# Kernel optimization log

Hardware: AMD Instinct MI355X
Metric: run time of the kernel (lower is better)

Reference implementation:

```python
import jax, jax.numpy as jnp
import numpy as np

DILATION = 6
KS = 3
N = KS * KS  # 9 kernel sample points
PAD = 1      # zero padding inside DeformConv2d
EPS = 1e-5


def conv2d(x, w, b=None, padding=0):
    out = jax.lax.conv_general_dilated(
        x, w, window_strides=(1, 1),
        padding=[(padding, padding), (padding, padding)],
        dimension_numbers=('NCHW', 'OIHW', 'NCHW'))
    if b is not None:
        out = out + b[None, :, None, None]
    return out


def batchnorm_train(x, gamma, beta):
    # training-mode BN (module default): batch statistics over (N,H,W)
    mean = x.mean(axis=(0, 2, 3), keepdims=True)
    var = x.var(axis=(0, 2, 3), keepdims=True)
    return gamma[None, :, None, None] * (x - mean) * jax.lax.rsqrt(var + EPS) + beta[None, :, None, None]


def deform_conv(x, p_w, p_b, m_w, m_b, d_w, d_b, w):
    b, c, h, wd = x.shape
    offset = conv2d(x, p_w, p_b, padding=1)                 # (b, 2N, h, w)
    m = jax.nn.sigmoid(conv2d(x, m_w, m_b, padding=1))      # (b, N, h, w) modulation
    s = 2.0 * jax.nn.sigmoid(conv2d(x, d_w, d_b, padding=1))  # (b,1,h,w) adaptive dilation scale (=1 at logit 0)
    xp = jnp.pad(x, ((0, 0), (0, 0), (PAD, PAD), (PAD, PAD)))
    Hp, Wp = h + 2 * PAD, wd + 2 * PAD
    # kernel grid p_n, row-major (kh, kw) to match conv weight layout
    rng = jnp.arange(-(KS - 1) // 2, (KS - 1) // 2 + 1, dtype=x.dtype)
    pn_x, pn_y = jnp.meshgrid(rng, rng, indexing='ij')
    pn_x, pn_y = pn_x.reshape(-1), pn_y.reshape(-1)          # (N,)
    # base sampling positions (offset by PAD into padded map)
    p0_x = jnp.arange(1, h + 1, dtype=x.dtype)[:, None, None]    # (h,1,1)
    p0_y = jnp.arange(1, wd + 1, dtype=x.dtype)[None, :, None]   # (1,w,1)
    off = offset.transpose(0, 2, 3, 1)   # (b,h,w,2N)
    s_ = s.transpose(0, 2, 3, 1)         # (b,h,w,1)
    px = p0_x + DILATION * s_ * pn_x + off[..., :N]   # (b,h,w,N)
    py = p0_y + DILATION * s_ * pn_y + off[..., N:]
    fx, fy = jnp.floor(px), jnp.floor(py)
    qx_lt = jnp.clip(fx, 0, Hp - 1).astype(jnp.int32)
    qy_lt = jnp.clip(fy, 0, Wp - 1).astype(jnp.int32)
    qx_rb = jnp.clip(fx + 1, 0, Hp - 1).astype(jnp.int32)
    qy_rb = jnp.clip(fy + 1, 0, Wp - 1).astype(jnp.int32)
    pxc = jnp.clip(px, 0, Hp - 1)
    pyc = jnp.clip(py, 0, Wp - 1)
    g_lt = (1 + (qx_lt - pxc)) * (1 + (qy_lt - pyc))
    g_rb = (1 - (qx_rb - pxc)) * (1 - (qy_rb - pyc))
    g_lb = (1 + (qx_lt - pxc)) * (1 - (qy_rb - pyc))
    g_rt = (1 - (qx_rb - pxc)) * (1 + (qy_lt - pyc))

    def gather(qx, qy):
        idx = (qx * Wp + qy).reshape(b, 1, -1)                    # (b,1,h*w*N)
        xf = xp.reshape(b, c, Hp * Wp)
        out = jnp.take_along_axis(xf, jnp.broadcast_to(idx, (b, c, idx.shape[-1])), axis=2)
        return out.reshape(b, c, h, wd, N)

    x_off = (g_lt[:, None] * gather(qx_lt, qy_lt)
             + g_rb[:, None] * gather(qx_rb, qy_rb)
             + g_lb[:, None] * gather(qx_lt, qy_rb)
             + g_rt[:, None] * gather(qx_rb, qy_lt))
    x_off = x_off * m.transpose(0, 2, 3, 1)[:, None]              # modulation
    # final 3x3 conv over gathered samples == contraction over (c, N)
    return jnp.einsum('bchwn,ocn->bohw', x_off, w.reshape(w.shape[0], c, N))


def setup_inputs() -> dict:
    key = jax.random.key(0)
    ks = jax.random.split(key, 12)
    cin, c1, c2 = 512, 256, 64
    b, h, w = 2, 96, 96
    def rn(k, shape, scale):
        return jax.random.normal(k, shape, dtype=jnp.float32) * scale
    return {
        'x': rn(ks[0], (b, cin, h, w), 1.0),
        'bn1_g': jnp.ones((cin,), jnp.float32),
        'bn1_b': jnp.zeros((cin,), jnp.float32),
        'conv1_w': rn(ks[1], (c1, cin, 1, 1), (1.0 / cin) ** 0.5),
        'conv1_b': jnp.zeros((c1,), jnp.float32),
        'bn2_g': jnp.ones((c1,), jnp.float32),
        'bn2_b': jnp.zeros((c1,), jnp.float32),
        'p_w': rn(ks[2], (2 * N, c1, 3, 3), 0.01),
        'p_b': jnp.zeros((2 * N,), jnp.float32),
        'm_w': rn(ks[3], (N, c1, 3, 3), 0.01),
        'm_b': jnp.zeros((N,), jnp.float32),
        'd_w': rn(ks[4], (1, c1, 3, 3), 0.01),
        'd_b': jnp.zeros((1,), jnp.float32),
        'dconv_w': rn(ks[5], (c2, c1, 3, 3), (1.0 / (c1 * 9)) ** 0.5),
    }


def reference(x, bn1_g, bn1_b, conv1_w, conv1_b, bn2_g, bn2_b,
              p_w, p_b, m_w, m_b, d_w, d_b, dconv_w):
    f = jax.nn.relu(batchnorm_train(x, bn1_g, bn1_b))
    f = conv2d(f, conv1_w, conv1_b)
    f = batchnorm_train(f, bn2_g, bn2_b)
    return deform_conv(f, p_w, p_b, m_w, m_b, d_w, d_b, dconv_w)
```

## Files before the change

kernel.cpp:

```cpp
#include <hip/hip_runtime.h>
#include <hip/hip_bf16.h>
#include <math.h>

#define BATCH 2
#define CIN 512
#define C1 256
#define C2 64
#define HH 96
#define WW 96
#define HWSZ 9216
#define NPIX 18432
#define HP 98
#define WP 98

typedef __attribute__((ext_vector_type(8))) short bf16x8;
typedef __attribute__((ext_vector_type(4))) short bf16x4;
typedef __attribute__((ext_vector_type(4))) float f32x4;
typedef __attribute__((ext_vector_type(4))) unsigned int u32x4;
typedef __attribute__((ext_vector_type(2))) unsigned int u32x2;
typedef unsigned short u16;
typedef unsigned int u32;

__device__ __forceinline__ float bfu2f(u16 u) {
  u32 v = ((u32)u) << 16; return __builtin_bit_cast(float, v);
}
__device__ __forceinline__ u16 f2bfu(float f) {
  return __builtin_bit_cast(u16, __float2bfloat16(f));
}
__device__ __forceinline__ float rd_any(const void* p, size_t i, int fl) {
  return fl ? bfu2f(((const u16*)p)[i]) : ((const float*)p)[i];
}
__device__ __forceinline__ int get_fl(const u32* g1raw) {
  return g1raw[0] != 0x3F800000u;
}
__device__ __forceinline__ bf16x8 lds_frag(const u16* p) {
  bf16x4 lo = *(const bf16x4*)p;
  bf16x4 hi = *(const bf16x4*)(p + 4);
  bf16x8 r;
  r[0] = lo[0]; r[1] = lo[1]; r[2] = lo[2]; r[3] = lo[3];
  r[4] = hi[0]; r[5] = hi[1]; r[6] = hi[2]; r[7] = hi[3];
  return r;
}
__device__ __forceinline__ void split4(const f32x4& v, u32x2& ph, u32x2& pl) {
  u16 h0 = f2bfu(v[0]), h1 = f2bfu(v[1]), h2 = f2bfu(v[2]), h3 = f2bfu(v[3]);
  u16 l0 = f2bfu(v[0] - bfu2f(h0)), l1 = f2bfu(v[1] - bfu2f(h1));
  u16 l2 = f2bfu(v[2] - bfu2f(h2)), l3 = f2bfu(v[3] - bfu2f(h3));
  ph = (u32x2){(u32)h0 | ((u32)h1 << 16), (u32)h2 | ((u32)h3 << 16)};
  pl = (u32x2){(u32)l0 | ((u32)l1 << 16), (u32)l2 | ((u32)l3 << 16)};
}

__global__ __launch_bounds__(256) void prep_kernel(
    const void* cw, const void* pw, const void* mw, const void* dw, const void* dcw,
    const void* cb, const void* g1, const void* b1, const void* g2, const void* b2,
    const void* pb, const void* mb, const void* db,
    u16* __restrict__ W1b, u16* __restrict__ W1l,
    u16* __restrict__ Wofa, u16* __restrict__ Wofal,
    u16* __restrict__ Wab, u16* __restrict__ Wabl,
    float* __restrict__ canon, float* __restrict__ statz) {
  int e = blockIdx.x * 256 + threadIdx.x;
  if (e >= 356380) return;
  int fl = get_fl((const u32*)g1);
  if (e < 131072) {
    float v = rd_any(cw, e, fl);
    u16 h = f2bfu(v);
    W1b[e] = h; W1l[e] = f2bfu(v - bfu2f(h));
  } else if (e < 204800) {
    int i = e - 131072;
    int tap = i >> 13; int r = i & 8191; int m = r >> 8; int c = r & 255;
    float v = 0.f;
    if (m < 18)       v = rd_any(pw, (size_t)(m * 256 + c) * 9 + tap, fl);
    else if (m < 27)  v = rd_any(mw, (size_t)((m - 18) * 256 + c) * 9 + tap, fl);
    else if (m == 27) v = rd_any(dw, (size_t)c * 9 + tap, fl);
    u16 h = f2bfu(v);
    Wofa[i] = h; Wofal[i] = f2bfu(v - bfu2f(h));
  } else if (e < 352256) {
    int i = e - 204800;
    int n = i >> 14; int r = i & 16383; int o = r >> 8; int c = r & 255;
    float v = rd_any(dcw, (size_t)(o * 256 + c) * 9 + n, fl);
    u16 h = f2bfu(v);
    Wab[i] = h; Wabl[i] = f2bfu(v - bfu2f(h));
  } else if (e < 354076) {
    int i = e - 352256;
    const void* src; int off;
    if      (i < 256)  { src = cb; off = i; }
    else if (i < 768)  { src = g1; off = i - 256; }
    else if (i < 1280) { src = b1; off = i - 768; }
    else if (i < 1536) { src = g2; off = i - 1280; }
    else if (i < 1792) { src = b2; off = i - 1536; }
    else if (i < 1810) { src = pb; off = i - 1792; }
    else if (i < 1819) { src = mb; off = i - 1810; }
    else               { src = db; off = i - 1819; }
    canon[i] = rd_any(src, off, fl);
  } else {
    statz[e - 354076] = 0.f;
  }
}

__global__ __launch_bounds__(256) void bn_stats_kernel(
    const void* __restrict__ x, const float* __restrict__ gamma,
    const float* __restrict__ beta, float* __restrict__ scale,
    float* __restrict__ shift, float* __restrict__ sums, float* __restrict__ sumsq,
    int* __restrict__ cnt, const u32* __restrict__ g1raw, int force, int C) {
  int c = blockIdx.x, part = blockIdx.y, tid = threadIdx.x;
  int fl = force ? 1 : get_fl(g1raw);
  int b = part >> 1, half = part & 1;
  size_t base = ((size_t)(b * C + c)) * HWSZ + half * (HWSZ / 2);
  float s = 0.f, q = 0.f;
  if (fl) {
    const u16* p = (const u16*)x + base;
    for (int i = tid; i < 576; i += 256) {
      u32x4 U = *(const u32x4*)(p + i * 8);
      #pragma unroll
      for (int k = 0; k < 4; ++k) {
        float v0 = bfu2f((u16)(U[k] & 0xffff));
        float v1 = bfu2f((u16)(U[k] >> 16));
        s += v0 + v1; q = fmaf(v0, v0, fmaf(v1, v1, q));
      }
    }
  } else {
    const float* p = (const float*)x + base;
    for (int i = tid; i < 1152; i += 256) {
      f32x4 v = *(const f32x4*)(p + i * 4);
      #pragma unroll
      for (int k = 0; k < 4; ++k) { s += v[k]; q = fmaf(v[k], v[k], q); }
    }
  }
  __shared__ float sh[512];
  sh[tid] = s; sh[tid + 256] = q;
  __syncthreads();
  for (int off = 128; off > 0; off >>= 1) {
    if (tid < off) { sh[tid] += sh[tid + off]; sh[tid + 256] += sh[tid + 256 + off]; }
    __syncthreads();
  }
  if (tid == 0) {
    atomicAdd(&sums[c], sh[0]);
    atomicAdd(&sumsq[c], sh[256]);
    __threadfence();
    int old = atomicAdd(&cnt[c], 1);
    if (old == 3) {
      float S = atomicAdd(&sums[c], 0.f);
      float Q = atomicAdd(&sumsq[c], 0.f);
      float mean = S * (1.f / (float)NPIX);
      float var  = fmaxf(Q * (1.f / (float)NPIX) - mean * mean, 0.f);
      float sc = gamma[c] * rsqrtf(var + 1e-5f);
      scale[c] = sc;
      shift[c] = beta[c] - mean * sc;
    }
  }
}

__global__ __launch_bounds__(256) void conv1x1_kernel(
    const void* __restrict__ x, const u16* __restrict__ W1b, const u16* __restrict__ W1l,
    const float* __restrict__ cb, const float* __restrict__ scale,
    const float* __restrict__ shift, const u32* __restrict__ g1raw,
    u16* __restrict__ f1) {
  __shared__ u16 Bh[2][64][68];
  __shared__ u16 Bl[2][64][68];
  int tid = threadIdx.x;
  int fl = get_fl(g1raw);
  int bxr = blockIdx.x;
  int bx = (bxr & 7) * 36 + (bxr >> 3);
  int p0 = bx * 64;
  int co0 = blockIdx.y * 128;
  int b = p0 / HWSZ;
  int hw0 = p0 % HWSZ;
  int lane = tid & 63, wv = tid >> 6, quad = lane >> 4, mr = lane & 15;
  int m0 = co0 + wv * 32;
  f32x4 acc[2][4];
  #pragma unroll
  for (int i = 0; i < 2; ++i)
    #pragma unroll
    for (int j = 0; j < 4; ++j) acc[i][j] = (f32x4){0.f, 0.f, 0.f, 0.f};

  int spx = tid & 63, cg = tid >> 6;
  int gpx = hw0 + spx;

  float pva[8], pvb[8];
  auto ISSUE = [&](int c0) {
    #pragma unroll
    for (int j = 0; j < 8; ++j) {
      int ci = c0 + cg * 16 + j * 2;
      if (fl) {
        const u16* xb = (const u16*)x;
        pva[j] = bfu2f(xb[((size_t)(b * CIN + ci)) * HWSZ + gpx]);
        pvb[j] = bfu2f(xb[((size_t)(b * CIN + ci + 1)) * HWSZ + gpx]);
      } else {
        const float* xf = (const float*)x;
        pva[j] = xf[((size_t)(b * CIN + ci)) * HWSZ + gpx];
        pvb[j] = xf[((size_t)(b * CIN + ci + 1)) * HWSZ + gpx];
      }
    }
  };
  auto COMBINE = [&](int buf, int c0) {
    #pragma unroll
    for (int j = 0; j < 8; ++j) {
      int ci = c0 + cg * 16 + j * 2;
      float v0 = fmaxf(fmaf(pva[j], scale[ci], shift[ci]), 0.f);
      float v1 = fmaxf(fmaf(pvb[j], scale[ci + 1], shift[ci + 1]), 0.f);
      u16 h0 = f2bfu(v0), h1 = f2bfu(v1);
      u16 l0 = f2bfu(v0 - bfu2f(h0)), l1 = f2bfu(v1 - bfu2f(h1));
      *(u32*)&Bh[buf][spx][cg * 16 + j * 2] = (u32)h0 | ((u32)h1 << 16);
      *(u32*)&Bl[buf][spx][cg * 16 + j * 2] = (u32)l0 | ((u32)l1 << 16);
    }
  };

  ISSUE(0);
  COMBINE(0, 0);
  for (int c8 = 0; c8 < 8; ++c8) {
    __syncthreads();
    if (c8 < 7) ISSUE((c8 + 1) * 64);
    int bsel = c8 & 1;
    int c0 = c8 * 64;
    #pragma unroll
    for (int kk2 = 0; kk2 < 2; ++kk2) {
      int kk = kk2 * 32;
      #pragma unroll
      for (int mf = 0; mf < 2; ++mf) {
        size_t wix = (size_t)(m0 + mf * 16 + mr) * CIN + c0 + kk + quad * 8;
        bf16x8 ah = *(const bf16x8*)(W1b + wix);
        bf16x8 al = *(const bf16x8*)(W1l + wix);
        #pragma unroll
        for (int nt = 0; nt < 4; ++nt) {
          bf16x8 bl = lds_frag(&Bl[bsel][nt * 16 + mr][kk + quad * 8]);
          bf16x8 bh = lds_frag(&Bh[bsel][nt * 16 + mr][kk + quad * 8]);
          acc[mf][nt] = __builtin_amdgcn_mfma_f32_16x16x32_bf16(ah, bl, acc[mf][nt], 0, 0, 0);
          acc[mf][nt] = __builtin_amdgcn_mfma_f32_16x16x32_bf16(al, bh, acc[mf][nt], 0, 0, 0);
          acc[mf][nt] = __builtin_amdgcn_mfma_f32_16x16x32_bf16(ah, bh, acc[mf][nt], 0, 0, 0);
        }
      }
    }
    if (c8 < 7) COMBINE(bsel ^ 1, (c8 + 1) * 64);
  }
  #pragma unroll
  for (int mf = 0; mf < 2; ++mf) {
    #pragma unroll
    for (int nt = 0; nt < 4; ++nt) {
      #pragma unroll
      for (int r = 0; r < 4; ++r) {
        int co = m0 + mf * 16 + quad * 4 + r;
        f1[((size_t)(b * C1 + co)) * HWSZ + hw0 + nt * 16 + mr] = f2bfu(acc[mf][nt][r] + cb[co]);
      }
    }
  }
}

__global__ __launch_bounds__(256) void bn2pad_kernel(
    const u16* __restrict__ f1, const float* __restrict__ scale,
    const float* __restrict__ shift, float* __restrict__ xpf) {
  int bid = blockIdx.x;
  int ht = bid % 144; int ct = (bid / 144) & 3; int b = bid / 576;
  int hw0 = ht * 64, c0 = ct * 64;
  __shared__ float t[64][65];
  int tid = threadIdx.x;
  #pragma unroll
  for (int it = 0; it < 16; ++it) {
    int e = it * 256 + tid;
    int p = e & 63, ci = e >> 6;
    float v = bfu2f(f1[((size_t)(b * C1 + c0 + ci)) * HWSZ + hw0 + p]);
    t[ci][p] = fmaf(v, scale[c0 + ci], shift[c0 + ci]);
  }
  __syncthreads();
  #pragma unroll
  for (int it = 0; it < 16; ++it) {
    int e = it * 256 + tid;
    int ci = e & 63, p = e >> 6;
    int hw = hw0 + p; int h = hw / WW; int w = hw % WW;
    xpf[(((size_t)(b * HP) + h + 1) * WP + w + 1) * C1 + c0 + ci] = t[ci][p];
  }
}

__global__ __launch_bounds__(256) void init_kernel(
    const u32* __restrict__ g1raw, void* __restrict__ outv,
    float* __restrict__ oscr, float* __restrict__ opart, float* __restrict__ xpf) {
  int i = blockIdx.x * 256 + threadIdx.x;
  if (i < 1179648) {
    if (get_fl(g1raw)) { ((u16*)outv)[i] = 0; oscr[i] = 0.f; }
    else               { ((float*)outv)[i] = 0.f; }
  } else if (i < 1769472) {
    opart[i - 1179648] = 0.f;
  } else {
    int k = i - 1769472;
    int ch = k & 255; int pxi = k >> 8;
    int bb = pxi / 388; int r = pxi % 388;
    int h, w;
    if (r < 98)      { h = 0;  w = r; }
    else if (r < 196){ h = 97; w = r - 98; }
    else if (r < 292){ h = r - 196 + 1; w = 0; }
    else             { h = r - 292 + 1; w = 97; }
    xpf[(((size_t)(bb * HP) + h) * WP + w) * C1 + ch] = 0.f;
  }
}

__global__ __launch_bounds__(256) void offconv_kernel(
    const float* __restrict__ xpf, const u16* __restrict__ Wofa, const u16* __restrict__ Wofal,
    const float* __restrict__ pbc, const float* __restrict__ mbc,
    const float* __restrict__ dbc, float* __restrict__ opart) {
  __shared__ u16 Vh[2][32][68];
  __shared__ u16 Vl[2][32][68];
  int tid = threadIdx.x;
  int bxr = blockIdx.x;
  int bx = (bxr & 7) * 72 + (bxr >> 3);
  int tg = blockIdx.y;
  int p0 = bx * 32;
  int b = p0 / HWSZ;
  int hw = p0 % HWSZ; int h0 = hw / WW; int w0 = hw % WW;
  int lane = tid & 63, wv = tid >> 6, quad = lane >> 4, mr = lane & 15;
  int m0 = (wv & 1) * 16;
  int ntile = wv >> 1;
  int srow = tid >> 4;
  int scol = (tid & 15) * 4;
  f32x4 acc = (f32x4){0.f, 0.f, 0.f, 0.f};

  f32x4 pv[2];
  auto ISSUE = [&](int it) {
    int tap = tg * 3 + (it >> 2);
    int th = tap / 3, tw = tap % 3;
    int c0 = (it & 3) * 64;
    const float* base = xpf + ((size_t)(b * HP + h0 + th) * WP + (w0 + tw)) * C1;
    #pragma unroll
    for (int pass = 0; pass < 2; ++pass) {
      int px = pass * 16 + srow;
      pv[pass] = *(const f32x4*)(base + (size_t)px * C1 + c0 + scol);
    }
  };
  auto COMBINE = [&](int buf) {
    #pragma unroll
    for (int pass = 0; pass < 2; ++pass) {
      int px = pass * 16 + srow;
      u32x2 ph, pl;
      split4(pv[pass], ph, pl);
      *(u32x2*)&Vh[buf][px][scol] = ph;
      *(u32x2*)&Vl[buf][px][scol] = pl;
    }
  };

  ISSUE(0);
  COMBINE(0);
  for (int it = 0; it < 12; ++it) {
    __syncthreads();
    if (it < 11) ISSUE(it + 1);
    int bsel = it & 1;
    int tap = tg * 3 + (it >> 2);
    int c0 = (it & 3) * 64;
    #pragma unroll
    for (int kk2 = 0; kk2 < 2; ++kk2) {
      int kof = kk2 * 32 + quad * 8;
      size_t wix = (size_t)(tap * 32 + m0 + mr) * C1 + c0 + kof;
      bf16x8 ah = *(const bf16x8*)(Wofa + wix);
      bf16x8 al = *(const bf16x8*)(Wofal + wix);
      bf16x8 bl = lds_frag(&Vl[bsel][ntile * 16 + mr][kof]);
      bf16x8 bh = lds_frag(&Vh[bsel][ntile * 16 + mr][kof]);
      acc = __builtin_amdgcn_mfma_f32_16x16x32_bf16(ah, bl, acc, 0, 0, 0);
      acc = __builtin_amdgcn_mfma_f32_16x16x32_bf16(al, bh, acc, 0, 0, 0);
      acc = __builtin_amdgcn_mfma_f32_16x16x32_bf16(ah, bh, acc, 0, 0, 0);
    }
    if (it < 11) COMBINE(bsel ^ 1);
  }
  int px = ntile * 16 + mr;
  #pragma unroll
  for (int r = 0; r < 4; ++r) {
    int m = m0 + quad * 4 + r;
    if (m < 28) {
      float v = acc[r];
      if (tg == 0) v += (m < 18) ? pbc[m] : ((m < 27) ? mbc[m - 18] : dbc[0]);
      atomicAdd(&opart[(size_t)m * NPIX + p0 + px], v);
    }
  }
}

__global__ __launch_bounds__(256) void deform_kernel(
    const float* __restrict__ xpf, const u16* __restrict__ Wab, const u16* __restrict__ Wabl,
    const float* __restrict__ opart, const u32* __restrict__ g1raw,
    float* __restrict__ oscr, void* __restrict__ outv) {
  __shared__ u16   Vh[2][64][68];
  __shared__ u16   Vl[2][64][68];
  __shared__ int   smi[4][64];
  __shared__ float smw[4][64];
  int tid = threadIdx.x;
  int bxr = blockIdx.x;
  int bx = (bxr & 7) * 36 + (bxr >> 3);
  int n = blockIdx.y;
  int p0 = bx * 64;
  int b = p0 / HWSZ;
  int hw0 = p0 % HWSZ;

  if (tid < 64) {
    int p = tid;
    int bp = p0 + p;
    int hw = hw0 + p; int h = hw / WW; int w = hw % WW;
    float offx = opart[(size_t)n * NPIX + bp];
    float offy = opart[(size_t)(9 + n) * NPIX + bp];
    float mlog = opart[(size_t)(18 + n) * NPIX + bp];
    float slog = opart[(size_t)27 * NPIX + bp];
    float mm = 1.f / (1.f + expf(-mlog));
    float s  = 2.f / (1.f + expf(-slog));
    float pnx = (float)(n / 3 - 1), pny = (float)(n % 3 - 1);
    float px = (float)(h + 1) + 6.f * s * pnx + offx;
    float py = (float)(w + 1) + 6.f * s * pny + offy;
    float fx = floorf(px), fy = floorf(py);
    float qxlt = fminf(fmaxf(fx, 0.f), 97.f);
    float qylt = fminf(fmaxf(fy, 0.f), 97.f);
    float qxrb = fminf(fmaxf(fx + 1.f, 0.f), 97.f);
    float qyrb = fminf(fmaxf(fy + 1.f, 0.f), 97.f);
    float pxc = fminf(fmaxf(px, 0.f), 97.f);
    float pyc = fminf(fmaxf(py, 0.f), 97.f);
    float glt = (1.f + (qxlt - pxc)) * (1.f + (qylt - pyc));
    float grb = (1.f - (qxrb - pxc)) * (1.f - (qyrb - pyc));
    float glb = (1.f + (qxlt - pxc)) * (1.f - (qyrb - pyc));
    float grt = (1.f - (qxrb - pxc)) * (1.f + (qylt - pyc));
    int ixlt = (int)qxlt, iylt = (int)qylt, ixrb = (int)qxrb, iyrb = (int)qyrb;
    int base = b * (HP * WP);
    smi[0][p] = base + ixlt * WP + iylt;  smw[0][p] = glt * mm;
    smi[1][p] = base + ixrb * WP + iyrb;  smw[1][p] = grb * mm;
    smi[2][p] = base + ixlt * WP + iyrb;  smw[2][p] = glb * mm;
    smi[3][p] = base + ixrb * WP + iylt;  smw[3][p] = grt * mm;
  }
  __syncthreads();

  int lane = tid & 63, wv = tid >> 6, quad = lane >> 4, mr = lane & 15;
  int m0 = wv * 16;
  int srow = tid >> 4;
  int scol = (tid & 15) * 4;
  f32x4 acc[4];
  #pragma unroll
  for (int i = 0; i < 4; ++i) acc[i] = (f32x4){0.f, 0.f, 0.f, 0.f};

  f32x4 pv[4][4];
  auto ISSUE = [&](int c0) {
    #pragma unroll
    for (int pass = 0; pass < 4; ++pass) {
      int px = pass * 16 + srow;
      #pragma unroll
      for (int k = 0; k < 4; ++k)
        pv[pass][k] = *(const f32x4*)(xpf + (size_t)smi[k][px] * C1 + c0 + scol);
    }
  };
  auto COMBINE = [&](int buf) {
    #pragma unroll
    for (int pass = 0; pass < 4; ++pass) {
      int px = pass * 16 + srow;
      float w0 = smw[0][px], w1 = smw[1][px], w2 = smw[2][px], w3 = smw[3][px];
      f32x4 vc;
      #pragma unroll
      for (int j = 0; j < 4; ++j)
        vc[j] = fmaf(w0, pv[pass][0][j],
                fmaf(w1, pv[pass][1][j],
                fmaf(w2, pv[pass][2][j], w3 * pv[pass][3][j])));
      u32x2 ph, pl;
      split4(vc, ph, pl);
      *(u32x2*)&Vh[buf][px][scol] = ph;
      *(u32x2*)&Vl[buf][px][scol] = pl;
    }
  };

  ISSUE(0);
  COMBINE(0);
  for (int c0i = 0; c0i < 4; ++c0i) {
    __syncthreads();
    if (c0i < 3) ISSUE((c0i + 1) * 64);
    int bsel = c0i & 1;
    int c0 = c0i * 64;
    #pragma unroll
    for (int kk2 = 0; kk2 < 2; ++kk2) {
      int kof = kk2 * 32 + quad * 8;
      size_t wix = (size_t)(n * C2 + m0 + mr) * C1 + c0 + kof;
      bf16x8 ah = *(const bf16x8*)(Wab + wix);
      bf16x8 al = *(const bf16x8*)(Wabl + wix);
      #pragma unroll
      for (int nt = 0; nt < 4; ++nt) {
        bf16x8 bl = lds_frag(&Vl[bsel][nt * 16 + mr][kof]);
        bf16x8 bh = lds_frag(&Vh[bsel][nt * 16 + mr][kof]);
        acc[nt] = __builtin_amdgcn_mfma_f32_16x16x32_bf16(ah, bl, acc[nt], 0, 0, 0);
        acc[nt] = __builtin_amdgcn_mfma_f32_16x16x32_bf16(al, bh, acc[nt], 0, 0, 0);
        acc[nt] = __builtin_amdgcn_mfma_f32_16x16x32_bf16(ah, bh, acc[nt], 0, 0, 0);
      }
    }
    if (c0i < 3) COMBINE(bsel ^ 1);
  }
  int fl = get_fl(g1raw);
  float* tgt = fl ? oscr : (float*)outv;
  #pragma unroll
  for (int nt = 0; nt < 4; ++nt) {
    #pragma unroll
    for (int r = 0; r < 4; ++r) {
      int o = m0 + quad * 4 + r;
      int hw = hw0 + nt * 16 + mr;
      atomicAdd(&tgt[((size_t)(b * C2 + o)) * HWSZ + hw], acc[nt][r]);
    }
  }
}

__global__ void cvt_out_kernel(const u32* __restrict__ g1raw,
                               const float* __restrict__ oscr, void* __restrict__ outv) {
  if (!get_fl(g1raw)) return;
  int i = blockIdx.x * 256 + threadIdx.x;
  ((u16*)outv)[i] = f2bfu(oscr[i]);
}

extern "C" void kernel_launch(void* const* d_in, const int* in_sizes, int n_in,
                              void* d_out, int out_size, void* d_ws, size_t ws_size,
                              hipStream_t stream) {
  const void* x       = d_in[0];
  const void* bn1_g   = d_in[1];
  const void* bn1_b   = d_in[2];
  const void* conv1_w = d_in[3];
  const void* conv1_b = d_in[4];
  const void* bn2_g   = d_in[5];
  const void* bn2_b   = d_in[6];
  const void* p_w     = d_in[7];
  const void* p_b     = d_in[8];
  const void* m_w     = d_in[9];
  const void* m_b     = d_in[10];
  const void* d_w     = d_in[11];
  const void* d_b     = d_in[12];
  const void* dconv_w = d_in[13];
  const u32* g1raw = (const u32*)bn1_g;

  float* ws = (float*)d_ws;
  float* canon = ws + 16;
  float* cbc = canon + 0;
  float* g1c = canon + 256;
  float* b1c = canon + 768;
  float* g2c = canon + 1280;
  float* b2c = canon + 1536;
  float* pbc = canon + 1792;
  float* mbc = canon + 1810;
  float* dbc = canon + 1819;
  float* scale1 = ws + 1840;
  float* shift1 = ws + 2352;
  float* scale2 = ws + 2864;
  float* shift2 = ws + 3120;
  float* statz  = ws + 3376;
  float* sums1  = statz;
  float* sumsq1 = statz + 512;
  int*   cnt1   = (int*)(statz + 1024);
  float* sums2  = statz + 1536;
  float* sumsq2 = statz + 1792;
  int*   cnt2   = (int*)(statz + 2048);
  u16* W1b   = (u16*)(ws + 5680);
  u16* W1l   = (u16*)(ws + 71216);
  u16* Wofa  = (u16*)(ws + 136752);
  u16* Wofal = (u16*)(ws + 173616);
  u16* Wab   = (u16*)(ws + 210480);
  u16* Wabl  = (u16*)(ws + 284208);
  u16* f1    = (u16*)(ws + 357936);
  float* oscr  = ws + 357936;
  float* opart = ws + 1537584;
  float* xpf   = ws + 2717232;

  prep_kernel<<<1393, 256, 0, stream>>>(conv1_w, p_w, m_w, d_w, dconv_w,
                                        conv1_b, bn1_g, bn1_b, bn2_g, bn2_b,
                                        p_b, m_b, d_b,
                                        W1b, W1l, Wofa, Wofal, Wab, Wabl, canon, statz);
  bn_stats_kernel<<<dim3(CIN, 4), 256, 0, stream>>>(x, g1c, b1c, scale1, shift1,
                                                    sums1, sumsq1, cnt1, g1raw, 0, CIN);
  conv1x1_kernel<<<dim3(288, 2), 256, 0, stream>>>(x, W1b, W1l, cbc, scale1, shift1, g1raw, f1);
  bn_stats_kernel<<<dim3(C1, 4), 256, 0, stream>>>(f1, g2c, b2c, scale2, shift2,
                                                   sums2, sumsq2, cnt2, g1raw, 1, C1);
  bn2pad_kernel<<<1152, 256, 0, stream>>>(f1, scale2, shift2, xpf);
  init_kernel<<<7688, 256, 0, stream>>>(g1raw, d_out, oscr, opart, xpf);
  offconv_kernel<<<dim3(576, 3), 256, 0, stream>>>(xpf, Wofa, Wofal, pbc, mbc, dbc, opart);
  deform_kernel<<<dim3(288, 9), 256, 0, stream>>>(xpf, Wab, Wabl, opart, g1raw, oscr, d_out);
  cvt_out_kernel<<<4608, 256, 0, stream>>>(g1raw, oscr, d_out);
}
```

Measured before the change: 308.4 us.

## Replace atomic accumulation with per-tap-group planes and in-block tap reduction

The offset conv now writes each of its three tap-group partial sums to a separate plane, and the deform kernel adds them up on read, so no atomics or zero-init are needed. The deform kernel loops over all 9 kernel taps inside one block of 32 pixels, so it writes the final output directly in the output dtype. This removes the output zeroing, the atomicAdds and the bf16 conversion kernel. In exchange the deform kernel has a smaller pixel tile, a longer serial 36-step loop and fewer blocks (576), which may lower parallelism.

```diff
diff --git a/kernel.cpp b/kernel.cpp
--- a/kernel.cpp
+++ b/kernel.cpp
@@ -12,6 +12,7 @@
 #define NPIX 18432
 #define HP 98
 #define WP 98
+#define PLSTRIDE 516096
 
 typedef __attribute__((ext_vector_type(8))) short bf16x8;
 typedef __attribute__((ext_vector_type(4))) short bf16x4;
@@ -269,32 +270,22 @@
   }
 }
 
-__global__ __launch_bounds__(256) void init_kernel(
-    const u32* __restrict__ g1raw, void* __restrict__ outv,
-    float* __restrict__ oscr, float* __restrict__ opart, float* __restrict__ xpf) {
-  int i = blockIdx.x * 256 + threadIdx.x;
-  if (i < 1179648) {
-    if (get_fl(g1raw)) { ((u16*)outv)[i] = 0; oscr[i] = 0.f; }
-    else               { ((float*)outv)[i] = 0.f; }
-  } else if (i < 1769472) {
-    opart[i - 1179648] = 0.f;
-  } else {
-    int k = i - 1769472;
-    int ch = k & 255; int pxi = k >> 8;
-    int bb = pxi / 388; int r = pxi % 388;
-    int h, w;
-    if (r < 98)      { h = 0;  w = r; }
-    else if (r < 196){ h = 97; w = r - 98; }
-    else if (r < 292){ h = r - 196 + 1; w = 0; }
-    else             { h = r - 292 + 1; w = 97; }
-    xpf[(((size_t)(bb * HP) + h) * WP + w) * C1 + ch] = 0.f;
-  }
+__global__ __launch_bounds__(256) void init_kernel(float* __restrict__ xpf) {
+  int k = blockIdx.x * 256 + threadIdx.x;
+  int ch = k & 255; int pxi = k >> 8;
+  int bb = pxi / 388; int r = pxi % 388;
+  int h, w;
+  if (r < 98)      { h = 0;  w = r; }
+  else if (r < 196){ h = 97; w = r - 98; }
+  else if (r < 292){ h = r - 196 + 1; w = 0; }
+  else             { h = r - 292 + 1; w = 97; }
+  xpf[(((size_t)(bb * HP) + h) * WP + w) * C1 + ch] = 0.f;
 }
 
 __global__ __launch_bounds__(256) void offconv_kernel(
     const float* __restrict__ xpf, const u16* __restrict__ Wofa, const u16* __restrict__ Wofal,
     const float* __restrict__ pbc, const float* __restrict__ mbc,
-    const float* __restrict__ dbc, float* __restrict__ opart) {
+    const float* __restrict__ dbc, float* __restrict__ opart3) {
   __shared__ u16 Vh[2][32][68];
   __shared__ u16 Vl[2][32][68];
   int tid = threadIdx.x;
@@ -356,6 +347,7 @@
     }
     if (it < 11) COMBINE(bsel ^ 1);
   }
+  float* plane = opart3 + (size_t)tg * PLSTRIDE;
   int px = ntile * 16 + mr;
   #pragma unroll
   for (int r = 0; r < 4; ++r) {
@@ -363,35 +355,42 @@
     if (m < 28) {
       float v = acc[r];
       if (tg == 0) v += (m < 18) ? pbc[m] : ((m < 27) ? mbc[m - 18] : dbc[0]);
-      atomicAdd(&opart[(size_t)m * NPIX + p0 + px], v);
+      plane[(size_t)m * NPIX + p0 + px] = v;
     }
   }
 }
 
 __global__ __launch_bounds__(256) void deform_kernel(
     const float* __restrict__ xpf, const u16* __restrict__ Wab, const u16* __restrict__ Wabl,
-    const float* __restrict__ opart, const u32* __restrict__ g1raw,
-    float* __restrict__ oscr, void* __restrict__ outv) {
-  __shared__ u16   Vh[2][64][68];
-  __shared__ u16   Vl[2][64][68];
-  __shared__ int   smi[4][64];
-  __shared__ float smw[4][64];
+    const float* __restrict__ opart3, const u32* __restrict__ g1raw,
+    void* __restrict__ outv) {
+  __shared__ u16   Vh[2][32][68];
+  __shared__ u16   Vl[2][32][68];
+  __shared__ int   smi[9][4][32];
+  __shared__ float smw[9][4][32];
   int tid = threadIdx.x;
   int bxr = blockIdx.x;
-  int bx = (bxr & 7) * 36 + (bxr >> 3);
-  int n = blockIdx.y;
-  int p0 = bx * 64;
+  int bx = (bxr & 7) * 72 + (bxr >> 3);
+  int p0 = bx * 32;
   int b = p0 / HWSZ;
   int hw0 = p0 % HWSZ;
 
-  if (tid < 64) {
-    int p = tid;
+  for (int e = tid; e < 288; e += 256) {
+    int n = e >> 5;
+    int p = e & 31;
     int bp = p0 + p;
     int hw = hw0 + p; int h = hw / WW; int w = hw % WW;
-    float offx = opart[(size_t)n * NPIX + bp];
-    float offy = opart[(size_t)(9 + n) * NPIX + bp];
-    float mlog = opart[(size_t)(18 + n) * NPIX + bp];
-    float slog = opart[(size_t)27 * NPIX + bp];
+    const float* P0 = opart3;
+    const float* P1 = opart3 + PLSTRIDE;
+    const float* P2 = opart3 + 2 * PLSTRIDE;
+    size_t iox = (size_t)n * NPIX + bp;
+    size_t ioy = (size_t)(9 + n) * NPIX + bp;
+    size_t iml = (size_t)(18 + n) * NPIX + bp;
+    size_t isl = (size_t)27 * NPIX + bp;
+    float offx = P0[iox] + P1[iox] + P2[iox];
+    float offy = P0[ioy] + P1[ioy] + P2[ioy];
+    float mlog = P0[iml] + P1[iml] + P2[iml];
+    float slog = P0[isl] + P1[isl] + P2[isl];
     float mm = 1.f / (1.f + expf(-mlog));
     float s  = 2.f / (1.f + expf(-slog));
     float pnx = (float)(n / 3 - 1), pny = (float)(n % 3 - 1);
@@ -410,10 +409,10 @@
     float grt = (1.f - (qxrb - pxc)) * (1.f + (qylt - pyc));
     int ixlt = (int)qxlt, iylt = (int)qylt, ixrb = (int)qxrb, iyrb = (int)qyrb;
     int base = b * (HP * WP);
-    smi[0][p] = base + ixlt * WP + iylt;  smw[0][p] = glt * mm;
-    smi[1][p] = base + ixrb * WP + iyrb;  smw[1][p] = grb * mm;
-    smi[2][p] = base + ixlt * WP + iyrb;  smw[2][p] = glb * mm;
-    smi[3][p] = base + ixrb * WP + iylt;  smw[3][p] = grt * mm;
+    smi[n][0][p] = base + ixlt * WP + iylt;  smw[n][0][p] = glt * mm;
+    smi[n][1][p] = base + ixrb * WP + iyrb;  smw[n][1][p] = grb * mm;
+    smi[n][2][p] = base + ixlt * WP + iyrb;  smw[n][2][p] = glb * mm;
+    smi[n][3][p] = base + ixrb * WP + iylt;  smw[n][3][p] = grt * mm;
   }
   __syncthreads();
 
@@ -421,25 +420,27 @@
   int m0 = wv * 16;
   int srow = tid >> 4;
   int scol = (tid & 15) * 4;
-  f32x4 acc[4];
-  #pragma unroll
-  for (int i = 0; i < 4; ++i) acc[i] = (f32x4){0.f, 0.f, 0.f, 0.f};
-
-  f32x4 pv[4][4];
-  auto ISSUE = [&](int c0) {
-    #pragma unroll
-    for (int pass = 0; pass < 4; ++pass) {
+  f32x4 acc[2];
+  acc[0] = (f32x4){0.f, 0.f, 0.f, 0.f};
+  acc[1] = (f32x4){0.f, 0.f, 0.f, 0.f};
+
+  f32x4 pv[2][4];
+  auto ISSUE = [&](int it) {
+    int n = it >> 2; int c0 = (it & 3) * 64;
+    #pragma unroll
+    for (int pass = 0; pass < 2; ++pass) {
       int px = pass * 16 + srow;
       #pragma unroll
       for (int k = 0; k < 4; ++k)
-        pv[pass][k] = *(const f32x4*)(xpf + (size_t)smi[k][px] * C1 + c0 + scol);
+        pv[pass][k] = *(const f32x4*)(xpf + (size_t)smi[n][k][px] * C1 + c0 + scol);
     }
   };
-  auto COMBINE = [&](int buf) {
-    #pragma unroll
-    for (int pass = 0; pass < 4; ++pass) {
+  auto COMBINE = [&](int buf, int it) {
+    int n = it >> 2;
+    #pragma unroll
+    for (int pass = 0; pass < 2; ++pass) {
       int px = pass * 16 + srow;
-      float w0 = smw[0][px], w1 = smw[1][px], w2 = smw[2][px], w3 = smw[3][px];
+      float w0 = smw[n][0][px], w1 = smw[n][1][px], w2 = smw[n][2][px], w3 = smw[n][3][px];
       f32x4 vc;
       #pragma unroll
       for (int j = 0; j < 4; ++j)
@@ -454,12 +455,12 @@
   };
 
   ISSUE(0);
-  COMBINE(0);
-  for (int c0i = 0; c0i < 4; ++c0i) {
+  COMBINE(0, 0);
+  for (int it = 0; it < 36; ++it) {
     __syncthreads();
-    if (c0i < 3) ISSUE((c0i + 1) * 64);
-    int bsel = c0i & 1;
-    int c0 = c0i * 64;
+    if (it < 35) ISSUE(it + 1);
+    int bsel = it & 1;
+    int n = it >> 2; int c0 = (it & 3) * 64;
     #pragma unroll
     for (int kk2 = 0; kk2 < 2; ++kk2) {
       int kof = kk2 * 32 + quad * 8;
@@ -467,7 +468,7 @@
       bf16x8 ah = *(const bf16x8*)(Wab + wix);
       bf16x8 al = *(const bf16x8*)(Wabl + wix);
       #pragma unroll
-      for (int nt = 0; nt < 4; ++nt) {
+      for (int nt = 0; nt < 2; ++nt) {
         bf16x8 bl = lds_frag(&Vl[bsel][nt * 16 + mr][kof]);
         bf16x8 bh = lds_frag(&Vh[bsel][nt * 16 + mr][kof]);
         acc[nt] = __builtin_amdgcn_mfma_f32_16x16x32_bf16(ah, bl, acc[nt], 0, 0, 0);
@@ -475,26 +476,20 @@
         acc[nt] = __builtin_amdgcn_mfma_f32_16x16x32_bf16(ah, bh, acc[nt], 0, 0, 0);
       }
     }
-    if (c0i < 3) COMBINE(bsel ^ 1);
+    if (it < 35) COMBINE(bsel ^ 1, it + 1);
   }
   int fl = get_fl(g1raw);
-  float* tgt = fl ? oscr : (float*)outv;
   #pragma unroll
-  for (int nt = 0; nt < 4; ++nt) {
+  for (int nt = 0; nt < 2; ++nt) {
     #pragma unroll
     for (int r = 0; r < 4; ++r) {
       int o = m0 + quad * 4 + r;
       int hw = hw0 + nt * 16 + mr;
-      atomicAdd(&tgt[((size_t)(b * C2 + o)) * HWSZ + hw], acc[nt][r]);
-    }
-  }
-}
-
-__global__ void cvt_out_kernel(const u32* __restrict__ g1raw,
-                               const float* __restrict__ oscr, void* __restrict__ outv) {
-  if (!get_fl(g1raw)) return;
-  int i = blockIdx.x * 256 + threadIdx.x;
-  ((u16*)outv)[i] = f2bfu(oscr[i]);
+      size_t oi = ((size_t)(b * C2 + o)) * HWSZ + hw;
+      if (fl) ((u16*)outv)[oi] = f2bfu(acc[nt][r]);
+      else    ((float*)outv)[oi] = acc[nt][r];
+    }
+  }
 }
 
 extern "C" void kernel_launch(void* const* d_in, const int* in_sizes, int n_in,
@@ -544,8 +539,7 @@
   u16* Wab   = (u16*)(ws + 210480);
   u16* Wabl  = (u16*)(ws + 284208);
   u16* f1    = (u16*)(ws + 357936);
-  float* oscr  = ws + 357936;
-  float* opart = ws + 1537584;
+  float* opart3 = ws + 357936;
   float* xpf   = ws + 2717232;
 
   prep_kernel<<<1393, 256, 0, stream>>>(conv1_w, p_w, m_w, d_w, dconv_w,
@@ -558,8 +552,7 @@
   bn_stats_kernel<<<dim3(C1, 4), 256, 0, stream>>>(f1, g2c, b2c, scale2, shift2,
                                                    sums2, sumsq2, cnt2, g1raw, 1, C1);
   bn2pad_kernel<<<1152, 256, 0, stream>>>(f1, scale2, shift2, xpf);
-  init_kernel<<<7688, 256, 0, stream>>>(g1raw, d_out, oscr, opart, xpf);
-  offconv_kernel<<<dim3(576, 3), 256, 0, stream>>>(xpf, Wofa, Wofal, pbc, mbc, dbc, opart);
-  deform_kernel<<<dim3(288, 9), 256, 0, stream>>>(xpf, Wab, Wabl, opart, g1raw, oscr, d_out);
-  cvt_out_kernel<<<4608, 256, 0, stream>>>(g1raw, oscr, d_out);
-}
+  init_kernel<<<776, 256, 0, stream>>>(xpf);
+  offconv_kernel<<<dim3(576, 3), 256, 0, stream>>>(xpf, Wofa, Wofal, pbc, mbc, dbc, opart3);
+  deform_kernel<<<576, 256, 0, stream>>>(xpf, Wab, Wabl, opart3, g1raw, d_out);
+}
```

New measurement: 332.6 us. 7.8% more time.
